# Performance work log

Hardware: AMD Instinct MI355X
Metric: run time of the kernel (lower is better)

## Reference

```python
import jax, jax.numpy as jnp
import numpy as np

N_LAYER = 4
N_HEAD = 16
N_EMBD = 1024
BLOCK = 1024
VOCAB = 100
TRANS = 16          # obs_dim + action_dim + 2 = 11 + 3 + 2
OBS_DIM = 11
ACT_DIM = 3
B, T = 2, 1024
VTOT = VOCAB * TRANS + 1  # token embedding rows
LN_EPS = 1e-5


def _layernorm(x, w, b):
    mu = jnp.mean(x, axis=-1, keepdims=True)
    var = jnp.var(x, axis=-1, keepdims=True)
    return (x - mu) * jax.lax.rsqrt(var + LN_EPS) * w + b


def _build_mask(t):
    # causal tril with every (joined_dim-1 mod joined_dim) column zeroed
    jd = OBS_DIM + ACT_DIM + 2  # 16
    m = jnp.tril(jnp.ones((t, t), dtype=bool))
    cols = jnp.arange(t)
    m = m & ((cols % jd) != (jd - 1))[None, :]
    return m  # [T, T] bool, True = keep


def setup_inputs() -> dict:
    key = jax.random.key(0)
    ks = jax.random.split(key, 24)
    C, L, F4 = N_EMBD, N_LAYER, 4 * N_EMBD
    g = lambda k, s: jax.random.normal(k, s, dtype=jnp.float32) * 0.02
    return {
        "tokens": jax.random.randint(ks[0], (B, T), 0, VTOT),
        "tok_emb": g(ks[1], (VTOT, C)),
        "pos_emb": g(ks[2], (1, BLOCK, C)),
        "Wq": g(ks[3], (L, C, C)), "bq": jnp.zeros((L, C), jnp.float32),
        "Wk": g(ks[4], (L, C, C)), "bk": jnp.zeros((L, C), jnp.float32),
        "Wv": g(ks[5], (L, C, C)), "bv": jnp.zeros((L, C), jnp.float32),
        "Wp": g(ks[6], (L, C, C)), "bp": jnp.zeros((L, C), jnp.float32),
        "ln1w": jnp.ones((L, C), jnp.float32), "ln1b": jnp.zeros((L, C), jnp.float32),
        "ln2w": jnp.ones((L, C), jnp.float32), "ln2b": jnp.zeros((L, C), jnp.float32),
        "W1": g(ks[7], (L, C, F4)), "b1": jnp.zeros((L, F4), jnp.float32),
        "W2": g(ks[8], (L, F4, C)), "b2": jnp.zeros((L, C), jnp.float32),
        "lnfw": jnp.ones((C,), jnp.float32), "lnfb": jnp.zeros((C,), jnp.float32),
        "head_w": g(ks[9], (TRANS, VOCAB + 1, C)),
    }


def _forward(tokens, tok_emb, pos_emb, Wq, bq, Wk, bk, Wv, bv, Wp, bp,
             ln1w, ln1b, ln2w, ln2b, W1, b1, W2, b2, lnfw, lnfb, head_w):
    b, t = tokens.shape
    C, H = N_EMBD, N_HEAD
    D = C // H
    scale = 1.0 / np.sqrt(D)
    mask = _build_mask(t)[None, None]  # [1,1,T,T]

    x = tok_emb[tokens] + pos_emb[:, :t, :]  # [B,T,C]
    for i in range(N_LAYER):
        h = _layernorm(x, ln1w[i], ln1b[i])
        q = (h @ Wq[i] + bq[i]).reshape(b, t, H, D).transpose(0, 2, 1, 3)
        k = (h @ Wk[i] + bk[i]).reshape(b, t, H, D).transpose(0, 2, 1, 3)
        v = (h @ Wv[i] + bv[i]).reshape(b, t, H, D).transpose(0, 2, 1, 3)
        att = jnp.einsum('bhtd,bhsd->bhts', q, k) * scale  # attn_bias=None => +0
        att = jnp.where(mask, att, -jnp.inf)
        att = jax.nn.softmax(att, axis=-1)
        y = jnp.einsum('bhts,bhsd->bhtd', att, v)
        y = y.transpose(0, 2, 1, 3).reshape(b, t, C)
        x = x + (y @ Wp[i] + bp[i])
        h2 = _layernorm(x, ln2w[i], ln2b[i])
        x = x + (jax.nn.gelu(h2 @ W1[i] + b1[i], approximate=False) @ W2[i] + b2[i])

    x = _layernorm(x, lnfw, lnfb)
    # pad_to_full_observation + EinLinear head
    n_pad = (TRANS - t % TRANS) % TRANS
    if n_pad:
        x = jnp.concatenate([x, jnp.zeros((b, n_pad, C), x.dtype)], axis=1)
    x_pad = x.reshape(-1, TRANS, C)                    # [b*n_states, TRANS, C]
    logits = jnp.einsum('eoi,bei->beo', head_w, x_pad)  # EinLinear, bias=False
    logits = logits.reshape(b, t + n_pad, VOCAB + 1)[:, :t]
    return logits


def reference(tokens, tok_emb, pos_emb, Wq, bq, Wk, bk, Wv, bv, Wp, bp,
              ln1w, ln1b, ln2w, ln2b, W1, b1, W2, b2, lnfw, lnfb, head_w):
    return _forward(tokens, tok_emb, pos_emb, Wq, bq, Wk, bk, Wv, bv, Wp, bp,
                    ln1w, ln1b, ln2w, ln2b, W1, b1, W2, b2, lnfw, lnfb, head_w)
```

## Files before the change

kernel.cpp:

```cpp
#include <hip/hip_runtime.h>
#include <hip/hip_bf16.h>
#include <math.h>

typedef unsigned short u16;
typedef __attribute__((ext_vector_type(8))) short short8;
typedef __attribute__((ext_vector_type(4))) short short4v;
typedef __attribute__((ext_vector_type(4))) float f32x4;

#define CDIM 1024
#define TDIM 1024
#define NROWS 2048
#define HEADS 16
#define HD 64
#define F4 4096

__device__ __forceinline__ u16 f2bf(float f) {
    union { float f; unsigned u; } v; v.f = f;
    unsigned r = v.u + 0x7fffu + ((v.u >> 16) & 1u);
    return (u16)(r >> 16);
}
__device__ __forceinline__ float bf2f(u16 h) {
    union { unsigned u; float f; } v; v.u = (unsigned)h << 16; return v.f;
}

__device__ __forceinline__ void gload_lds16(const void* g, void* lds) {
    __builtin_amdgcn_global_load_lds(
        (const __attribute__((address_space(1))) unsigned int*)g,
        (__attribute__((address_space(3))) unsigned int*)lds,
        16, 0, 0);
}

__device__ __forceinline__ void tile_map(int& bx, int& by, int& bz)
{
    const int gx = gridDim.x, gy = gridDim.y;
    const int fid = blockIdx.x + gx * (blockIdx.y + gy * blockIdx.z);
    const int nwg = gx * gy * gridDim.z;
    const int q = nwg >> 3, r = nwg & 7;
    const int xcd = fid & 7, t = fid >> 3;
    const int n = ((xcd < r) ? xcd * (q + 1) : r * (q + 1) + (xcd - r) * q) + t;
    const int nxy = gx * gy;
    bz = n / nxy;
    const int xy = n - bz * nxy;
    const int per_group = gx << 3;
    const int grp = xy / per_group;
    const int in = xy - grp * per_group;
    const int y0 = grp << 3;
    const int rem = gy - y0;
    const int gh = rem < 8 ? rem : 8;
    by = y0 + (in % gh);
    bx = in / gh;
}

__global__ __launch_bounds__(256)
void embed_k(const int* __restrict__ tok, const float* __restrict__ te,
             const float* __restrict__ pe, float* __restrict__ X)
{
    const int row = blockIdx.x;
    const int t = row & (TDIM - 1);
    const int tk = tok[row];
    const int c = threadIdx.x * 4;
    float4 a = *reinterpret_cast<const float4*>(te + (size_t)tk * CDIM + c);
    float4 b = *reinterpret_cast<const float4*>(pe + (size_t)t * CDIM + c);
    a.x += b.x; a.y += b.y; a.z += b.z; a.w += b.w;
    *reinterpret_cast<float4*>(X + (size_t)row * CDIM + c) = a;
}

template<bool BF16OUT>
__global__ __launch_bounds__(256)
void ln_k(const float* __restrict__ X, const float* __restrict__ g,
          const float* __restrict__ be, void* __restrict__ outp)
{
    __shared__ float red[4], red2[4];
    const int row = blockIdx.x, tid = threadIdx.x;
    const float* xr = X + (size_t)row * CDIM;
    const int c = tid * 4;
    float4 xv = *reinterpret_cast<const float4*>(xr + c);
    float s  = xv.x + xv.y + xv.z + xv.w;
    float s2 = xv.x*xv.x + xv.y*xv.y + xv.z*xv.z + xv.w*xv.w;
    #pragma unroll
    for (int off = 32; off; off >>= 1) {
        s  += __shfl_xor(s, off);
        s2 += __shfl_xor(s2, off);
    }
    if ((tid & 63) == 0) { red[tid >> 6] = s; red2[tid >> 6] = s2; }
    __syncthreads();
    const float ts  = red[0] + red[1] + red[2] + red[3];
    const float ts2 = red2[0] + red2[1] + red2[2] + red2[3];
    const float mu  = ts * (1.0f / CDIM);
    const float var = ts2 * (1.0f / CDIM) - mu * mu;
    const float rs  = rsqrtf(var + 1e-5f);
    float4 gv = *reinterpret_cast<const float4*>(g + c);
    float4 bv = *reinterpret_cast<const float4*>(be + c);
    float o0 = (xv.x - mu) * rs * gv.x + bv.x;
    float o1 = (xv.y - mu) * rs * gv.y + bv.y;
    float o2 = (xv.z - mu) * rs * gv.z + bv.z;
    float o3 = (xv.w - mu) * rs * gv.w + bv.w;
    if (BF16OUT) {
        u16 tmp[4] = { f2bf(o0), f2bf(o1), f2bf(o2), f2bf(o3) };
        u16* o = (u16*)outp + (size_t)row * CDIM + c;
        *reinterpret_cast<uint2*>(o) = *reinterpret_cast<const uint2*>(tmp);
    } else {
        float4 ov = { o0, o1, o2, o3 };
        *reinterpret_cast<float4*>((float*)outp + (size_t)row * CDIM + c) = ov;
    }
}

template<bool BF16OUT, int NZ>
__global__ __launch_bounds__(256)
void ln_red_k(float* __restrict__ X, const float* __restrict__ P,
              const float* __restrict__ g, const float* __restrict__ be,
              void* __restrict__ outp)
{
    __shared__ float red[4], red2[4];
    const int row = blockIdx.x, tid = threadIdx.x;
    const int c = tid * 4;
    float4 xv = *reinterpret_cast<const float4*>(X + (size_t)row * CDIM + c);
    #pragma unroll
    for (int z = 0; z < NZ; ++z) {
        float4 pv = *reinterpret_cast<const float4*>(P + ((size_t)z * NROWS + row) * CDIM + c);
        xv.x += pv.x; xv.y += pv.y; xv.z += pv.z; xv.w += pv.w;
    }
    *reinterpret_cast<float4*>(X + (size_t)row * CDIM + c) = xv;
    float s  = xv.x + xv.y + xv.z + xv.w;
    float s2 = xv.x*xv.x + xv.y*xv.y + xv.z*xv.z + xv.w*xv.w;
    #pragma unroll
    for (int off = 32; off; off >>= 1) {
        s  += __shfl_xor(s, off);
        s2 += __shfl_xor(s2, off);
    }
    if ((tid & 63) == 0) { red[tid >> 6] = s; red2[tid >> 6] = s2; }
    __syncthreads();
    const float ts  = red[0] + red[1] + red[2] + red[3];
    const float ts2 = red2[0] + red2[1] + red2[2] + red2[3];
    const float mu  = ts * (1.0f / CDIM);
    const float var = ts2 * (1.0f / CDIM) - mu * mu;
    const float rs  = rsqrtf(var + 1e-5f);
    float4 gv = *reinterpret_cast<const float4*>(g + c);
    float4 bv = *reinterpret_cast<const float4*>(be + c);
    float o0 = (xv.x - mu) * rs * gv.x + bv.x;
    float o1 = (xv.y - mu) * rs * gv.y + bv.y;
    float o2 = (xv.z - mu) * rs * gv.z + bv.z;
    float o3 = (xv.w - mu) * rs * gv.w + bv.w;
    if (BF16OUT) {
        u16 tmp[4] = { f2bf(o0), f2bf(o1), f2bf(o2), f2bf(o3) };
        u16* o = (u16*)outp + (size_t)row * CDIM + c;
        *reinterpret_cast<uint2*>(o) = *reinterpret_cast<const uint2*>(tmp);
    } else {
        float4 ov = { o0, o1, o2, o3 };
        *reinterpret_cast<float4*>((float*)outp + (size_t)row * CDIM + c) = ov;
    }
}

__global__ __launch_bounds__(256)
void convT_k(const float* __restrict__ W, u16* __restrict__ Wt,
             const int K, const int N)
{
    __shared__ u16 s[64][72];
    const int k0 = blockIdx.y * 64, n0 = blockIdx.x * 64;
    const int tr = threadIdx.x >> 4, tc = (threadIdx.x & 15) * 4;
    #pragma unroll
    for (int i = 0; i < 4; ++i) {
        int r = tr + i * 16;
        float4 w = *reinterpret_cast<const float4*>(W + (size_t)(k0 + r) * N + n0 + tc);
        s[r][tc + 0] = f2bf(w.x); s[r][tc + 1] = f2bf(w.y);
        s[r][tc + 2] = f2bf(w.z); s[r][tc + 3] = f2bf(w.w);
    }
    __syncthreads();
    #pragma unroll
    for (int i = 0; i < 4; ++i) {
        int n = tr + i * 16;
        u16 tmp[4];
        #pragma unroll
        for (int e = 0; e < 4; ++e) tmp[e] = s[tc + e][n];
        *reinterpret_cast<uint2*>(Wt + (size_t)(n0 + n) * K + k0 + tc) =
            *reinterpret_cast<const uint2*>(tmp);
    }
}

__global__ __launch_bounds__(256)
void pack_bias_k(const float* __restrict__ a, const float* __restrict__ b,
                 const float* __restrict__ c, float* __restrict__ o)
{
    const int i = threadIdx.x * 4;
    const float* s = blockIdx.x == 0 ? a : blockIdx.x == 1 ? b : c;
    *reinterpret_cast<float4*>(o + (size_t)blockIdx.x * 1024 + i) =
        *reinterpret_cast<const float4*>(s + i);
}

template<int EPI>
__global__ __launch_bounds__(256, 2)
void gemm_bt(const u16* __restrict__ A, const u16* __restrict__ Bt,
             const float* __restrict__ bias, u16* __restrict__ outb,
             float* __restrict__ resid, u16* __restrict__ vtout,
             const int N, const int K, const int KCH)
{
    __shared__ __align__(16) u16 sA[2][2][128 * 32];
    __shared__ __align__(16) u16 sB[2][2][128 * 32];
    const int tid = threadIdx.x;
    const int lane = tid & 63, wv = tid >> 6;
    int bx, by, bz;
    tile_map(bx, by, bz);
    const int m0 = by * 128, n0 = bx * 128;
    const int kbeg = bz * KCH, kend = kbeg + KCH;
    const int fr = lane & 15, fq = lane >> 4;
    const int wm = wv & 1, wn = wv >> 1;
    const int srow = lane >> 2, schunk = (lane & 3) * 8;
    f32x4 acc[4][4] = {};

    auto stage = [&](int k0, int buf) {
        #pragma unroll
        for (int kk = 0; kk < 2; ++kk)
            #pragma unroll
            for (int i = 0; i < 2; ++i) {
                const int reg = i * 4 + wv;
                gload_lds16(A  + (size_t)(m0 + reg * 16 + srow) * K + k0 + kk * 32 + schunk,
                            &sA[buf][kk][reg * 512]);
                gload_lds16(Bt + (size_t)(n0 + reg * 16 + srow) * K + k0 + kk * 32 + schunk,
                            &sB[buf][kk][reg * 512]);
            }
    };

    stage(kbeg, 0);
    int cur = 0;
    for (int k0 = kbeg; k0 < kend; k0 += 64) {
        __syncthreads();
        if (k0 + 64 < kend) stage(k0 + 64, cur ^ 1);
        #pragma unroll
        for (int kk = 0; kk < 2; ++kk) {
            short8 af[4], bf[4];
            #pragma unroll
            for (int mi = 0; mi < 4; ++mi)
                af[mi] = *reinterpret_cast<const short8*>(
                    &sA[cur][kk][(wm * 64 + mi * 16 + fr) * 32 + fq * 8]);
            #pragma unroll
            for (int nj = 0; nj < 4; ++nj)
                bf[nj] = *reinterpret_cast<const short8*>(
                    &sB[cur][kk][(wn * 64 + nj * 16 + fr) * 32 + fq * 8]);
            #pragma unroll
            for (int mi = 0; mi < 4; ++mi)
                #pragma unroll
                for (int nj = 0; nj < 4; ++nj)
                    acc[mi][nj] = __builtin_amdgcn_mfma_f32_16x16x32_bf16(af[mi], bf[nj], acc[mi][nj], 0, 0, 0);
        }
        cur ^= 1;
    }

    #pragma unroll
    for (int nj = 0; nj < 4; ++nj) {
        const int col = n0 + wn * 64 + nj * 16 + fr;
        const float bias_v = (EPI == 2 && bz != 0) ? 0.0f : bias[col];
        #pragma unroll
        for (int mi = 0; mi < 4; ++mi) {
            const int rowb = m0 + wm * 64 + mi * 16 + fq * 4;
            if (EPI == 0 && vtout != nullptr && col >= 2048) {
                const int bidx = rowb >> 10, t = rowb & 1023, hd = col - 2048;
                u16 t4[4];
                #pragma unroll
                for (int r = 0; r < 4; ++r) t4[r] = f2bf(acc[mi][nj][r] + bias_v);
                *reinterpret_cast<uint2*>(
                    vtout + ((size_t)(bidx * 16 + (hd >> 6)) * 64 + (hd & 63)) * 1024 + t) =
                    *reinterpret_cast<const uint2*>(t4);
            } else {
                #pragma unroll
                for (int r = 0; r < 4; ++r) {
                    const int row = rowb + r;
                    float cv = acc[mi][nj][r] + bias_v;
                    if (EPI == 0) {
                        outb[(size_t)row * N + col] = f2bf(cv);
                    } else if (EPI == 1) {
                        float gl = 0.5f * cv * (1.0f + erff(cv * 0.70710678118654752f));
                        outb[(size_t)row * N + col] = f2bf(gl);
                    } else {
                        resid[((size_t)bz * NROWS + row) * N + col] = cv;
                    }
                }
            }
        }
    }
}

__global__ __launch_bounds__(256, 4)
void attn_k(const u16* __restrict__ QKV, const u16* __restrict__ VT,
            float* __restrict__ po, float* __restrict__ plsum)
{
    __shared__ __align__(16) u16 sK[2][64][72];
    __shared__ __align__(16) u16 sV[2][64][72];
    const int tid = threadIdx.x, lane = tid & 63, wv = tid >> 6;
    const int fr = lane & 15, fq = lane >> 4;
    int bx, by, bz;
    tile_map(bx, by, bz);
    const int qt = bx, h = by, b = bz >> 1, sc = bz & 1;
    const int q0 = qt * 64;
    const int nt = qt + 1, h1 = (nt + 1) >> 1;
    const int stbeg = sc ? h1 : 0, stend = sc ? nt : h1;
    const u16* Qb = QKV + (size_t)b * TDIM * 3072 + h * HD;
    const u16* Vb = VT + ((size_t)(b * HEADS + h) * HD) * TDIM;
    const int r0 = tid >> 3, c0 = (tid & 7) * 8;

    const u16* qp = Qb + (size_t)(q0 + wv * 16 + fr) * 3072 + fq * 8;
    short8 aQ0 = *reinterpret_cast<const short8*>(qp);
    short8 aQ1 = *reinterpret_cast<const short8*>(qp + 32);

    f32x4 o[4] = {};
    float lsum = 0.0f;
    int cur = 0;

    if (stbeg < stend) {
        #pragma unroll
        for (int i = 0; i < 2; ++i) {
            const int r = r0 + i * 32;
            *reinterpret_cast<uint4*>(&sK[0][r][c0]) =
                *reinterpret_cast<const uint4*>(Qb + 1024 + (size_t)(stbeg * 64 + r) * 3072 + c0);
            *reinterpret_cast<uint4*>(&sV[0][r][c0]) =
                *reinterpret_cast<const uint4*>(Vb + (size_t)r * TDIM + stbeg * 64 + c0);
        }
        __syncthreads();
    }

    for (int st = stbeg; st < stend; ++st) {
        const int s0 = st * 64;
        const bool pf = (st + 1) < stend;
        uint4 pk[2], pv[2];
        if (pf) {
            #pragma unroll
            for (int i = 0; i < 2; ++i) {
                const int r = r0 + i * 32;
                pk[i] = *reinterpret_cast<const uint4*>(Qb + 1024 + (size_t)(s0 + 64 + r) * 3072 + c0);
                pv[i] = *reinterpret_cast<const uint4*>(Vb + (size_t)r * TDIM + s0 + 64 + c0);
            }
        }
        f32x4 sacc[4] = {};
        #pragma unroll
        for (int j = 0; j < 4; ++j) {
            short8 k0f = *reinterpret_cast<const short8*>(&sK[cur][j * 16 + fr][fq * 8]);
            sacc[j] = __builtin_amdgcn_mfma_f32_16x16x32_bf16(k0f, aQ0, sacc[j], 0, 0, 0);
            short8 k1f = *reinterpret_cast<const short8*>(&sK[cur][j * 16 + fr][32 + fq * 8]);
            sacc[j] = __builtin_amdgcn_mfma_f32_16x16x32_bf16(k1f, aQ1, sacc[j], 0, 0, 0);
        }
        const int qrow = q0 + wv * 16 + fr;
        u16 pb[4][4];
        #pragma unroll
        for (int j = 0; j < 4; ++j)
            #pragma unroll
            for (int r = 0; r < 4; ++r) {
                const int scol = s0 + j * 16 + fq * 4 + r;
                const bool keep = (scol <= qrow) && ((scol & 15) != 15);
                const float p = keep ? __expf(sacc[j][r] * 0.125f) : 0.0f;
                const u16 hb = f2bf(p);
                pb[j][r] = hb;
                lsum += bf2f(hb);
            }
        union { unsigned u[4]; short8 v; } a0, a1;
        a0.u[0] = (unsigned)pb[0][0] | ((unsigned)pb[0][1] << 16);
        a0.u[1] = (unsigned)pb[0][2] | ((unsigned)pb[0][3] << 16);
        a0.u[2] = (unsigned)pb[1][0] | ((unsigned)pb[1][1] << 16);
        a0.u[3] = (unsigned)pb[1][2] | ((unsigned)pb[1][3] << 16);
        a1.u[0] = (unsigned)pb[2][0] | ((unsigned)pb[2][1] << 16);
        a1.u[1] = (unsigned)pb[2][2] | ((unsigned)pb[2][3] << 16);
        a1.u[2] = (unsigned)pb[3][0] | ((unsigned)pb[3][1] << 16);
        a1.u[3] = (unsigned)pb[3][2] | ((unsigned)pb[3][3] << 16);
        #pragma unroll
        for (int j = 0; j < 4; ++j) {
            const u16* vrow = &sV[cur][j * 16 + fr][0];
            short4v v0 = *reinterpret_cast<const short4v*>(vrow + fq * 4);
            short4v v1 = *reinterpret_cast<const short4v*>(vrow + 16 + fq * 4);
            short8 bV0 = __builtin_shufflevector(v0, v1, 0, 1, 2, 3, 4, 5, 6, 7);
            o[j] = __builtin_amdgcn_mfma_f32_16x16x32_bf16(a0.v, bV0, o[j], 0, 0, 0);
            short4v v2 = *reinterpret_cast<const short4v*>(vrow + 32 + fq * 4);
            short4v v3 = *reinterpret_cast<const short4v*>(vrow + 48 + fq * 4);
            short8 bV1 = __builtin_shufflevector(v2, v3, 0, 1, 2, 3, 4, 5, 6, 7);
            o[j] = __builtin_amdgcn_mfma_f32_16x16x32_bf16(a1.v, bV1, o[j], 0, 0, 0);
        }
        if (pf) {
            #pragma unroll
            for (int i = 0; i < 2; ++i) {
                const int r = r0 + i * 32;
                *reinterpret_cast<uint4*>(&sK[cur ^ 1][r][c0]) = pk[i];
                *reinterpret_cast<uint4*>(&sV[cur ^ 1][r][c0]) = pv[i];
            }
            __syncthreads();
            cur ^= 1;
        }
    }

    lsum += __shfl_xor(lsum, 16);
    lsum += __shfl_xor(lsum, 32);

    const int tl = (bz * 16 + h) * 16 + qt;
    float* pt = po + (size_t)tl * 4096;
    #pragma unroll
    for (int j = 0; j < 4; ++j)
        #pragma unroll
        for (int r = 0; r < 4; ++r)
            pt[(wv * 16 + fq * 4 + r) * 64 + j * 16 + fr] = o[j][r];
    if (fq == 0) plsum[(size_t)tl * 64 + wv * 16 + fr] = lsum;
}

__global__ __launch_bounds__(256)
void attn_comb_k(const float* __restrict__ po, const float* __restrict__ plsum,
                 u16* __restrict__ Y)
{
    const int qt = blockIdx.x, h = blockIdx.y, b = blockIdx.z;
    const int t0 = ((b * 2 + 0) * 16 + h) * 16 + qt;
    const int t1 = ((b * 2 + 1) * 16 + h) * 16 + qt;
    const float* p0 = po + (size_t)t0 * 4096;
    const float* p1 = po + (size_t)t1 * 4096;
    const float* l0 = plsum + (size_t)t0 * 64;
    const float* l1 = plsum + (size_t)t1 * 64;
    #pragma unroll
    for (int i = 0; i < 4; ++i) {
        const int f4 = threadIdx.x + i * 256;
        const int q = f4 >> 4, d4 = (f4 & 15) * 4;
        float4 a = *reinterpret_cast<const float4*>(p0 + f4 * 4);
        float4 c = *reinterpret_cast<const float4*>(p1 + f4 * 4);
        const float rl = 1.0f / (l0[q] + l1[q]);
        u16 t4[4] = { f2bf((a.x + c.x) * rl), f2bf((a.y + c.y) * rl),
                      f2bf((a.z + c.z) * rl), f2bf((a.w + c.w) * rl) };
        *reinterpret_cast<uint2*>(
            Y + ((size_t)(b * TDIM + qt * 64 + q)) * CDIM + h * HD + d4) =
            *reinterpret_cast<const uint2*>(t4);
    }
}

__global__ __launch_bounds__(256)
void head_k(const float* __restrict__ Xf, const float* __restrict__ HW,
            float* __restrict__ out)
{
    int bx, by, bz;
    tile_map(bx, by, bz);
    const int e = by, b = bz;
    const int lane = threadIdx.x & 63, w = threadIdx.x >> 6;
    const int p = e + 16 * (bx * 4 + w);
    const size_t rowi = (size_t)b * 1024 + p;
    const float* xr = Xf + rowi * CDIM;
    float4 xa[4];
    #pragma unroll
    for (int i = 0; i < 4; ++i)
        xa[i] = *reinterpret_cast<const float4*>(xr + lane * 4 + i * 256);
    const float* wb = HW + (size_t)e * 101 * CDIM;
    float* orow = out + rowi * 101;
    for (int o = 0; o < 101; o += 2) {
        const int o2 = o + 1 < 101 ? o + 1 : 100;
        const float* wr0 = wb + (size_t)o * CDIM;
        const float* wr1 = wb + (size_t)o2 * CDIM;
        float s0 = 0.0f, s1 = 0.0f;
        #pragma unroll
        for (int i = 0; i < 4; ++i) {
            float4 w0 = *reinterpret_cast<const float4*>(wr0 + lane * 4 + i * 256);
            float4 w1 = *reinterpret_cast<const float4*>(wr1 + lane * 4 + i * 256);
            s0 += xa[i].x * w0.x + xa[i].y * w0.y + xa[i].z * w0.z + xa[i].w * w0.w;
            s1 += xa[i].x * w1.x + xa[i].y * w1.y + xa[i].z * w1.z + xa[i].w * w1.w;
        }
        #pragma unroll
        for (int off = 32; off; off >>= 1) {
            s0 += __shfl_xor(s0, off);
            s1 += __shfl_xor(s1, off);
        }
        if (lane == 0) {
            orow[o] = s0;
            if (o + 1 < 101) orow[o + 1] = s1;
        }
    }
}

extern "C" void kernel_launch(void* const* d_in, const int* in_sizes, int n_in,
                              void* d_out, int out_size, void* d_ws, size_t ws_size,
                              hipStream_t stream)
{
    const int*   tokens = (const int*)  d_in[0];
    const float* tok_emb= (const float*)d_in[1];
    const float* pos_emb= (const float*)d_in[2];
    const float* Wq = (const float*)d_in[3];
    const float* bq = (const float*)d_in[4];
    const float* Wk = (const float*)d_in[5];
    const float* bk = (const float*)d_in[6];
    const float* Wv = (const float*)d_in[7];
    const float* bv = (const float*)d_in[8];
    const float* Wp = (const float*)d_in[9];
    const float* bp = (const float*)d_in[10];
    const float* ln1w = (const float*)d_in[11];
    const float* ln1b = (const float*)d_in[12];
    const float* ln2w = (const float*)d_in[13];
    const float* ln2b = (const float*)d_in[14];
    const float* W1 = (const float*)d_in[15];
    const float* b1 = (const float*)d_in[16];
    const float* W2 = (const float*)d_in[17];
    const float* b2 = (const float*)d_in[18];
    const float* lnfw = (const float*)d_in[19];
    const float* lnfb = (const float*)d_in[20];
    const float* head_w = (const float*)d_in[21];
    float* out = (float*)d_out;

    char* ws = (char*)d_ws;
    float* x    = (float*)(ws);
    u16*   hbuf = (u16*)  (ws + (8u  << 20));
    u16*   yb   = (u16*)  (ws + (8u  << 20));
    u16*   qkv  = (u16*)  (ws + (12u << 20));
    u16*   vt   = (u16*)  (ws + (24u << 20));
    u16*   mid  = (u16*)  (ws + (12u << 20));
    float* hf   = (float*)(ws + (12u << 20));
    u16*   wbuf = (u16*)  (ws + (28u << 20));
    float* pbuf = (float*)(ws + (36u << 20));
    float* po   = (float*)(ws + (36u << 20));
    float* plsum= (float*)(ws + (53u << 20));
    float* bbuf = (float*)(ws + (68u << 20));

    embed_k<<<NROWS, 256, 0, stream>>>(tokens, tok_emb, pos_emb, x);

    for (int l = 0; l < 4; ++l) {
        const size_t wo = (size_t)l * CDIM * CDIM;
        convT_k<<<dim3(16, 16), 256, 0, stream>>>(Wq + wo, wbuf + 0u * CDIM * CDIM, CDIM, CDIM);
        convT_k<<<dim3(16, 16), 256, 0, stream>>>(Wk + wo, wbuf + 1u * CDIM * CDIM, CDIM, CDIM);
        convT_k<<<dim3(16, 16), 256, 0, stream>>>(Wv + wo, wbuf + 2u * CDIM * CDIM, CDIM, CDIM);
        pack_bias_k<<<3, 256, 0, stream>>>(bq + l * CDIM, bk + l * CDIM, bv + l * CDIM, bbuf);

        if (l == 0)
            ln_k<true><<<NROWS, 256, 0, stream>>>(x, ln1w, ln1b, hbuf);
        else
            ln_red_k<true, 4><<<NROWS, 256, 0, stream>>>(x, pbuf, ln1w + l * CDIM, ln1b + l * CDIM, hbuf);
        gemm_bt<0><<<dim3(24, 16, 1), 256, 0, stream>>>(hbuf, wbuf, bbuf, qkv, nullptr, vt, 3072, CDIM, CDIM);
        attn_k<<<dim3(16, HEADS, 4), 256, 0, stream>>>(qkv, vt, po, plsum);
        attn_comb_k<<<dim3(16, HEADS, 2), 256, 0, stream>>>(po, plsum, yb);

        convT_k<<<dim3(16, 16), 256, 0, stream>>>(Wp + wo, wbuf, CDIM, CDIM);
        gemm_bt<2><<<dim3(8, 16, 2), 256, 0, stream>>>(yb, wbuf, bp + l * CDIM, nullptr, pbuf, nullptr, CDIM, CDIM, 512);

        ln_red_k<true, 2><<<NROWS, 256, 0, stream>>>(x, pbuf, ln2w + l * CDIM, ln2b + l * CDIM, hbuf);
        convT_k<<<dim3(64, 16), 256, 0, stream>>>(W1 + (size_t)l * CDIM * F4, wbuf, CDIM, F4);
        gemm_bt<1><<<dim3(32, 16, 1), 256, 0, stream>>>(hbuf, wbuf, b1 + l * F4, mid, nullptr, nullptr, F4, CDIM, CDIM);
        convT_k<<<dim3(16, 64), 256, 0, stream>>>(W2 + (size_t)l * F4 * CDIM, wbuf, F4, CDIM);
        gemm_bt<2><<<dim3(8, 16, 4), 256, 0, stream>>>(mid, wbuf, b2 + l * CDIM, nullptr, pbuf, nullptr, CDIM, F4, CDIM);
    }

    ln_red_k<false, 4><<<NROWS, 256, 0, stream>>>(x, pbuf, lnfw, lnfb, hf);
    head_k<<<dim3(16, 16, 2), 256, 0, stream>>>(hf, head_w, out);
}
```

Before: 980.9 us.

## Run EinLinear head on MFMA with split-bf16 (hi/lo) emulated fp32 GEMM

Replaces the scalar fp32 head kernel with a batched MFMA GEMM. The final layernorm writes activations as bf16 hi/lo pairs grouped by head index, and the head weights are likewise split into hi/lo. A K=3072 concatenation (hi*hi + lo*hi + hi*lo) recovers near-fp32 accuracy. Split-K partials are summed in a small reduction kernel. This trades extra launches and a larger padded workspace (101 outputs padded to 128) for removing the slow, bandwidth-bound CUDA-core dot products.

```diff
diff --git a/kernel.cpp b/kernel.cpp
--- a/kernel.cpp
+++ b/kernel.cpp
@@ -105,7 +105,7 @@
     }
 }
 
-template<bool BF16OUT, int NZ>
+template<int MODE, int NZ>
 __global__ __launch_bounds__(256)
 void ln_red_k(float* __restrict__ X, const float* __restrict__ P,
               const float* __restrict__ g, const float* __restrict__ be,
@@ -120,7 +120,8 @@
         float4 pv = *reinterpret_cast<const float4*>(P + ((size_t)z * NROWS + row) * CDIM + c);
         xv.x += pv.x; xv.y += pv.y; xv.z += pv.z; xv.w += pv.w;
     }
-    *reinterpret_cast<float4*>(X + (size_t)row * CDIM + c) = xv;
+    if (MODE != 2)
+        *reinterpret_cast<float4*>(X + (size_t)row * CDIM + c) = xv;
     float s  = xv.x + xv.y + xv.z + xv.w;
     float s2 = xv.x*xv.x + xv.y*xv.y + xv.z*xv.z + xv.w*xv.w;
     #pragma unroll
@@ -141,13 +142,20 @@
     float o1 = (xv.y - mu) * rs * gv.y + bv.y;
     float o2 = (xv.z - mu) * rs * gv.z + bv.z;
     float o3 = (xv.w - mu) * rs * gv.w + bv.w;
-    if (BF16OUT) {
+    if (MODE == 0) {
         u16 tmp[4] = { f2bf(o0), f2bf(o1), f2bf(o2), f2bf(o3) };
         u16* o = (u16*)outp + (size_t)row * CDIM + c;
         *reinterpret_cast<uint2*>(o) = *reinterpret_cast<const uint2*>(tmp);
     } else {
-        float4 ov = { o0, o1, o2, o3 };
-        *reinterpret_cast<float4*>((float*)outp + (size_t)row * CDIM + c) = ov;
+        u16 hi[4] = { f2bf(o0), f2bf(o1), f2bf(o2), f2bf(o3) };
+        u16 lo[4] = { f2bf(o0 - bf2f(hi[0])), f2bf(o1 - bf2f(hi[1])),
+                      f2bf(o2 - bf2f(hi[2])), f2bf(o3 - bf2f(hi[3])) };
+        const int b = row >> 10, p = row & 1023;
+        const int e = p & 15, slot = p >> 4;
+        u16* ar = (u16*)outp + (size_t)(e * 128 + b * 64 + slot) * 3072;
+        *reinterpret_cast<uint2*>(ar + c)        = *reinterpret_cast<const uint2*>(hi);
+        *reinterpret_cast<uint2*>(ar + 1024 + c) = *reinterpret_cast<const uint2*>(lo);
+        *reinterpret_cast<uint2*>(ar + 2048 + c) = *reinterpret_cast<const uint2*>(hi);
     }
 }
 
@@ -175,6 +183,24 @@
         *reinterpret_cast<uint2*>(Wt + (size_t)(n0 + n) * K + k0 + tc) =
             *reinterpret_cast<const uint2*>(tmp);
     }
+}
+
+__global__ __launch_bounds__(256)
+void conv_head_k(const float* __restrict__ HW, u16* __restrict__ Wt)
+{
+    const int o = blockIdx.x, e = blockIdx.y;
+    const int c = threadIdx.x * 4;
+    u16 hi[4] = {0, 0, 0, 0}, lo[4] = {0, 0, 0, 0};
+    if (o < 101) {
+        float4 w = *reinterpret_cast<const float4*>(HW + ((size_t)e * 101 + o) * 1024 + c);
+        hi[0] = f2bf(w.x); hi[1] = f2bf(w.y); hi[2] = f2bf(w.z); hi[3] = f2bf(w.w);
+        lo[0] = f2bf(w.x - bf2f(hi[0])); lo[1] = f2bf(w.y - bf2f(hi[1]));
+        lo[2] = f2bf(w.z - bf2f(hi[2])); lo[3] = f2bf(w.w - bf2f(hi[3]));
+    }
+    u16* wr = Wt + (size_t)(e * 128 + o) * 3072;
+    *reinterpret_cast<uint2*>(wr + c)        = *reinterpret_cast<const uint2*>(hi);
+    *reinterpret_cast<uint2*>(wr + 1024 + c) = *reinterpret_cast<const uint2*>(hi);
+    *reinterpret_cast<uint2*>(wr + 2048 + c) = *reinterpret_cast<const uint2*>(lo);
 }
 
 __global__ __launch_bounds__(256)
@@ -205,6 +231,7 @@
     const int fr = lane & 15, fq = lane >> 4;
     const int wm = wv & 1, wn = wv >> 1;
     const int srow = lane >> 2, schunk = (lane & 3) * 8;
+    const u16* Bt2 = (EPI == 3) ? Bt + (size_t)by * 128 * K : Bt;
     f32x4 acc[4][4] = {};
 
     auto stage = [&](int k0, int buf) {
@@ -215,7 +242,7 @@
                 const int reg = i * 4 + wv;
                 gload_lds16(A  + (size_t)(m0 + reg * 16 + srow) * K + k0 + kk * 32 + schunk,
                             &sA[buf][kk][reg * 512]);
-                gload_lds16(Bt + (size_t)(n0 + reg * 16 + srow) * K + k0 + kk * 32 + schunk,
+                gload_lds16(Bt2 + (size_t)(n0 + reg * 16 + srow) * K + k0 + kk * 32 + schunk,
                             &sB[buf][kk][reg * 512]);
             }
     };
@@ -248,7 +275,8 @@
     #pragma unroll
     for (int nj = 0; nj < 4; ++nj) {
         const int col = n0 + wn * 64 + nj * 16 + fr;
-        const float bias_v = (EPI == 2 && bz != 0) ? 0.0f : bias[col];
+        const float bias_v = (EPI == 3) ? 0.0f
+                             : (EPI == 2 && bz != 0) ? 0.0f : bias[col];
         #pragma unroll
         for (int mi = 0; mi < 4; ++mi) {
             const int rowb = m0 + wm * 64 + mi * 16 + fq * 4;
@@ -270,13 +298,29 @@
                     } else if (EPI == 1) {
                         float gl = 0.5f * cv * (1.0f + erff(cv * 0.70710678118654752f));
                         outb[(size_t)row * N + col] = f2bf(gl);
+                    } else if (EPI == 2) {
+                        resid[((size_t)bz * NROWS + row) * N + col] = cv;
                     } else {
-                        resid[((size_t)bz * NROWS + row) * N + col] = cv;
+                        resid[((size_t)bz * NROWS + row) * 128 + col] = cv;
                     }
                 }
             }
         }
     }
+}
+
+__global__ __launch_bounds__(128)
+void head_red_k(const float* __restrict__ P, float* __restrict__ out)
+{
+    const int pr = blockIdx.x;
+    const int col = threadIdx.x;
+    const int e = pr >> 7, rem = pr & 127, b = rem >> 6, slot = rem & 63;
+    float s = 0.0f;
+    #pragma unroll
+    for (int z = 0; z < 8; ++z)
+        s += P[((size_t)z * NROWS + pr) * 128 + col];
+    if (col < 101)
+        out[((size_t)(b << 10) + (slot << 4) + e) * 101 + col] = s;
 }
 
 __global__ __launch_bounds__(256, 4)
@@ -419,47 +463,6 @@
         *reinterpret_cast<uint2*>(
             Y + ((size_t)(b * TDIM + qt * 64 + q)) * CDIM + h * HD + d4) =
             *reinterpret_cast<const uint2*>(t4);
-    }
-}
-
-__global__ __launch_bounds__(256)
-void head_k(const float* __restrict__ Xf, const float* __restrict__ HW,
-            float* __restrict__ out)
-{
-    int bx, by, bz;
-    tile_map(bx, by, bz);
-    const int e = by, b = bz;
-    const int lane = threadIdx.x & 63, w = threadIdx.x >> 6;
-    const int p = e + 16 * (bx * 4 + w);
-    const size_t rowi = (size_t)b * 1024 + p;
-    const float* xr = Xf + rowi * CDIM;
-    float4 xa[4];
-    #pragma unroll
-    for (int i = 0; i < 4; ++i)
-        xa[i] = *reinterpret_cast<const float4*>(xr + lane * 4 + i * 256);
-    const float* wb = HW + (size_t)e * 101 * CDIM;
-    float* orow = out + rowi * 101;
-    for (int o = 0; o < 101; o += 2) {
-        const int o2 = o + 1 < 101 ? o + 1 : 100;
-        const float* wr0 = wb + (size_t)o * CDIM;
-        const float* wr1 = wb + (size_t)o2 * CDIM;
-        float s0 = 0.0f, s1 = 0.0f;
-        #pragma unroll
-        for (int i = 0; i < 4; ++i) {
-            float4 w0 = *reinterpret_cast<const float4*>(wr0 + lane * 4 + i * 256);
-            float4 w1 = *reinterpret_cast<const float4*>(wr1 + lane * 4 + i * 256);
-            s0 += xa[i].x * w0.x + xa[i].y * w0.y + xa[i].z * w0.z + xa[i].w * w0.w;
-            s1 += xa[i].x * w1.x + xa[i].y * w1.y + xa[i].z * w1.z + xa[i].w * w1.w;
-        }
-        #pragma unroll
-        for (int off = 32; off; off >>= 1) {
-            s0 += __shfl_xor(s0, off);
-            s1 += __shfl_xor(s1, off);
-        }
-        if (lane == 0) {
-            orow[o] = s0;
-            if (o + 1 < 101) orow[o + 1] = s1;
-        }
     }
 }
 
@@ -493,14 +496,16 @@
 
     char* ws = (char*)d_ws;
     float* x    = (float*)(ws);
+    float* hpart= (float*)(ws);
     u16*   hbuf = (u16*)  (ws + (8u  << 20));
     u16*   yb   = (u16*)  (ws + (8u  << 20));
     u16*   qkv  = (u16*)  (ws + (12u << 20));
+    u16*   xg   = (u16*)  (ws + (12u << 20));
     u16*   vt   = (u16*)  (ws + (24u << 20));
     u16*   mid  = (u16*)  (ws + (12u << 20));
-    float* hf   = (float*)(ws + (12u << 20));
     u16*   wbuf = (u16*)  (ws + (28u << 20));
     float* pbuf = (float*)(ws + (36u << 20));
+    u16*   whp  = (u16*)  (ws + (36u << 20));
     float* po   = (float*)(ws + (36u << 20));
     float* plsum= (float*)(ws + (53u << 20));
     float* bbuf = (float*)(ws + (68u << 20));
@@ -517,7 +522,7 @@
         if (l == 0)
             ln_k<true><<<NROWS, 256, 0, stream>>>(x, ln1w, ln1b, hbuf);
         else
-            ln_red_k<true, 4><<<NROWS, 256, 0, stream>>>(x, pbuf, ln1w + l * CDIM, ln1b + l * CDIM, hbuf);
+            ln_red_k<0, 4><<<NROWS, 256, 0, stream>>>(x, pbuf, ln1w + l * CDIM, ln1b + l * CDIM, hbuf);
         gemm_bt<0><<<dim3(24, 16, 1), 256, 0, stream>>>(hbuf, wbuf, bbuf, qkv, nullptr, vt, 3072, CDIM, CDIM);
         attn_k<<<dim3(16, HEADS, 4), 256, 0, stream>>>(qkv, vt, po, plsum);
         attn_comb_k<<<dim3(16, HEADS, 2), 256, 0, stream>>>(po, plsum, yb);
@@ -525,13 +530,15 @@
         convT_k<<<dim3(16, 16), 256, 0, stream>>>(Wp + wo, wbuf, CDIM, CDIM);
         gemm_bt<2><<<dim3(8, 16, 2), 256, 0, stream>>>(yb, wbuf, bp + l * CDIM, nullptr, pbuf, nullptr, CDIM, CDIM, 512);
 
-        ln_red_k<true, 2><<<NROWS, 256, 0, stream>>>(x, pbuf, ln2w + l * CDIM, ln2b + l * CDIM, hbuf);
+        ln_red_k<0, 2><<<NROWS, 256, 0, stream>>>(x, pbuf, ln2w + l * CDIM, ln2b + l * CDIM, hbuf);
         convT_k<<<dim3(64, 16), 256, 0, stream>>>(W1 + (size_t)l * CDIM * F4, wbuf, CDIM, F4);
         gemm_bt<1><<<dim3(32, 16, 1), 256, 0, stream>>>(hbuf, wbuf, b1 + l * F4, mid, nullptr, nullptr, F4, CDIM, CDIM);
         convT_k<<<dim3(16, 64), 256, 0, stream>>>(W2 + (size_t)l * F4 * CDIM, wbuf, F4, CDIM);
         gemm_bt<2><<<dim3(8, 16, 4), 256, 0, stream>>>(mid, wbuf, b2 + l * CDIM, nullptr, pbuf, nullptr, CDIM, F4, CDIM);
     }
 
-    ln_red_k<false, 4><<<NROWS, 256, 0, stream>>>(x, pbuf, lnfw, lnfb, hf);
-    head_k<<<dim3(16, 16, 2), 256, 0, stream>>>(hf, head_w, out);
-}
+    ln_red_k<2, 4><<<NROWS, 256, 0, stream>>>(x, pbuf, lnfw, lnfb, xg);
+    conv_head_k<<<dim3(128, 16), 256, 0, stream>>>(head_w, whp);
+    gemm_bt<3><<<dim3(1, 16, 8), 256, 0, stream>>>(xg, whp, nullptr, nullptr, hpart, nullptr, 128, 3072, 384);
+    head_red_k<<<NROWS, 128, 0, stream>>>(hpart, out);
+}
```

New measurement: 956.5 us. 1.03x faster.
